# Kernel tuning notes

Hardware: AMD Instinct MI355X
Metric: run time of the kernel (lower is better)

## Reference

```python
import jax, jax.numpy as jnp
import numpy as np

B, N, E, D, L = 64, 128, 2048, 128, 4  # graphs, nodes/graph, edges/graph, channels, gnn layers
T = B * N  # total batched nodes


def setup_inputs() -> dict:
    key = jax.random.key(0)
    ks = jax.random.split(key, 16)
    s = 1.0 / np.sqrt(D)
    sc = 1.0 / np.sqrt(2 * D)
    inp = {
        "x": jax.random.normal(ks[0], (B, N, D), jnp.float32),
        "edges": jax.random.randint(ks[1], (B, 2, E), 0, N, dtype=jnp.int32),
        "Wg": jax.random.normal(ks[2], (L, D, D), jnp.float32) * s,
        "bg": jnp.zeros((L, D), jnp.float32),
        "Wq": jax.random.normal(ks[3], (D, D), jnp.float32) * s,
        "bq": jnp.zeros((D,), jnp.float32),
        "Wk": jax.random.normal(ks[4], (D, D), jnp.float32) * s,
        "bk": jnp.zeros((D,), jnp.float32),
        "Wv": jax.random.normal(ks[5], (D, D), jnp.float32) * s,
        "bv": jnp.zeros((D,), jnp.float32),
        "Wo": jax.random.normal(ks[6], (D, D), jnp.float32) * s,
        "bo": jnp.zeros((D,), jnp.float32),
        "Wc": jax.random.normal(ks[7], (2 * D, D), jnp.float32) * sc,
        "bc": jnp.zeros((D,), jnp.float32),
    }
    return inp


def _batched_edges(edges):
    # offset per-graph edge indices into the flat [T] node space, add self-loops
    off = (jnp.arange(B, dtype=edges.dtype) * N)[:, None]
    src = (edges[:, 0, :] + off).reshape(-1)
    dst = (edges[:, 1, :] + off).reshape(-1)
    loops = jnp.arange(T, dtype=edges.dtype)
    src = jnp.concatenate([src, loops])
    dst = jnp.concatenate([dst, loops])
    return src, dst


def reference(x, edges, Wg, bg, Wq, bq, Wk, bk, Wv, bv, Wo, bo, Wc, bc):
    xf = x.reshape(T, D)  # flat batched node features (torch_geo_batch.x)
    src, dst = _batched_edges(edges)
    # GCN symmetric normalization with self-loops: deg >= 1
    deg = jax.ops.segment_sum(jnp.ones(src.shape, xf.dtype), dst, num_segments=T)
    norm = jax.lax.rsqrt(deg)
    coef = (norm[src] * norm[dst])[:, None]
    # n_layers of GCNConv + tanh
    h = xf
    for l in range(L):
        m = h @ Wg[l]  # [T, D]
        h = jax.ops.segment_sum(m[src] * coef, dst, num_segments=T) + bg[l]
        h = jnp.tanh(h)
    batch_embedding = h.reshape(B, N, D)
    # DoubleHeadedAttention on the ORIGINAL batched input x; both inputs are
    # identical so the two attention heads compute the same tensor.
    q = xf @ Wq + bq
    k = xf @ Wk + bk
    v = xf @ Wv + bv
    attn = jax.nn.softmax(q @ k.T, axis=-1)  # [T, T]
    attended = (attn @ v) @ Wo + bo  # output_layer, == attended_input1 == attended_input2
    combined = jnp.concatenate([attended, attended], axis=-1)  # [T, 2D]
    att_output = combined @ Wc + bc  # combination_layer
    return jnp.concatenate([batch_embedding, att_output.reshape(B, N, D)], axis=-1)
```

## Files before the change

### kernel.cpp

```cpp
#include <hip/hip_runtime.h>
#include <math.h>

#define TT 8192
#define DD 128
#define GB 64
#define GN 128
#define GE 2048

#define WS_WG16    0u
#define WS_W2      (644u<<10)
#define WS_B2      (708u<<10)
#define WS_Q16     (1u<<20)
#define WS_K16     (3u<<20)
#define WS_VT      (5u<<20)
#define WS_OPART   (7u<<20)
#define WS_PM      (23u<<20)
#define WS_PL      ((23u<<20)+(256u<<10))

typedef _Float16 hfrag  __attribute__((ext_vector_type(8)));
typedef _Float16 h4     __attribute__((ext_vector_type(4)));
typedef float    ffrag  __attribute__((ext_vector_type(4)));

#define MFMA16(a,b,c) __builtin_amdgcn_mfma_f32_16x16x32_f16((a),(b),(c),0,0,0)

typedef __attribute__((address_space(1))) unsigned int gu32_t;
typedef __attribute__((address_space(3))) unsigned int lu32_t;
#define GLOAD16(gp, lp) __builtin_amdgcn_global_load_lds((gu32_t*)(const void*)(gp), (lu32_t*)(void*)(lp), 16, 0, 0)

__device__ __forceinline__ int fidx(int r_, int c_) {
  return (((r_>>4)*4 + (c_>>5))*64 + (r_&15) + 16*((c_>>3)&3))*8 + (c_&7);
}

__device__ __forceinline__ float tanh_fast(float x) {
  float e = __expf(2.f*x);
  return 1.f - 2.f/(e+1.f);
}

__global__ __launch_bounds__(512) void k_prep(const float* __restrict__ Wg,
                                              const float* __restrict__ Wo, const float* __restrict__ bo,
                                              const float* __restrict__ Wc, const float* __restrict__ bc,
                                              _Float16* __restrict__ wg16,
                                              float* __restrict__ W2, float* __restrict__ b2) {
  __shared__ float Wcs[128*128];
  const int tid = threadIdx.x;
  const int bid = blockIdx.x;
  if (bid < 4) {
    #pragma unroll
    for (int i=0;i<32;++i){
      int i2 = i*512 + tid;
      Wcs[i2] = Wc[i2] + Wc[i2 + 16384];
    }
    __syncthreads();
    const int r  = tid>>4;
    const int c0 = (tid&15)*8;
    const int ig = bid*32 + r;
    float acc[8];
    #pragma unroll
    for (int m=0;m<8;++m) acc[m]=0.f;
    for (int k=0;k<128;++k){
      float wo = Wo[ig*DD + k];
      #pragma unroll
      for (int m=0;m<8;++m) acc[m] += wo*Wcs[k*128 + c0 + m];
    }
    #pragma unroll
    for (int m=0;m<8;++m) W2[ig*DD + c0 + m] = acc[m];
    if (bid == 0){
      __syncthreads();
      if (tid < 128){
        float s = bc[tid];
        for (int k=0;k<128;++k) s += bo[k]*Wcs[k*128 + tid];
        b2[tid] = s;
      }
    }
  } else {
    const int l = bid - 4;
    const float* Wl = Wg + l*DD*DD;
    _Float16* dst = wg16 + l*16384;
    #pragma unroll
    for (int i=0;i<8;++i){
      int i4 = i*512 + tid;
      int k = i4>>5, i0 = (i4&31)<<2;
      float4 v = *(const float4*)&Wl[k*DD + i0];
      dst[fidx(i0+0,k)] = (_Float16)v.x;
      dst[fidx(i0+1,k)] = (_Float16)v.y;
      dst[fidx(i0+2,k)] = (_Float16)v.z;
      dst[fidx(i0+3,k)] = (_Float16)v.w;
    }
  }
}

__global__ __launch_bounds__(512,1) void fused_pre(
    const float* __restrict__ x, const int* __restrict__ edges,
    const _Float16* __restrict__ wg16, const float* __restrict__ bg,
    const float* __restrict__ Wq, const float* __restrict__ bq_,
    const float* __restrict__ Wk, const float* __restrict__ bk_,
    const float* __restrict__ Wv, const float* __restrict__ bv_,
    _Float16* __restrict__ q16, _Float16* __restrict__ k16, _Float16* __restrict__ vT,
    float* __restrict__ out)
{
  __shared__ __align__(16) char Lm[135168];
  const int tid  = threadIdx.x;
  const int bid  = blockIdx.x;

  if (bid < 64) {
    float*    Af   = (float*)Lm;
    _Float16* W16f = (_Float16*)Lm;
    _Float16* m16  = (_Float16*)(Lm + 32768);
    _Float16* h16  = (_Float16*)(Lm + 65536);
    _Float16* A16  = (_Float16*)(Lm + 98304);
    int*      cnt  = (int*)(Lm + 131072);
    float*    nrm  = (float*)(Lm + 131584);

    const int lane = tid & 63;
    const int w8   = tid >> 6;
    const int l15  = lane & 15;
    const int g    = lane >> 4;
    const int wi   = w8 >> 2;
    const int wj   = w8 & 3;
    const int b    = bid;
    const int* eg  = edges + b*2*GE;

    #pragma unroll
    for (int i=0;i<8;++i) ((float4*)Af)[i*512 + tid] = (float4){0.f,0.f,0.f,0.f};
    if (tid < 128) cnt[tid] = 0;
    __syncthreads();
    #pragma unroll
    for (int i=0;i<4;++i) atomicAdd(&cnt[eg[GE + i*512 + tid]], 1);
    __syncthreads();
    if (tid < 128) nrm[tid] = rsqrtf(1.f + (float)cnt[tid]);
    __syncthreads();
    #pragma unroll
    for (int i=0;i<4;++i){
      int s = eg[i*512 + tid], d = eg[GE + i*512 + tid];
      atomicAdd(&Af[d*128 + s], nrm[s]*nrm[d]);
    }
    __syncthreads();
    if (tid < 128) Af[tid*128 + tid] += nrm[tid]*nrm[tid];
    __syncthreads();
    #pragma unroll
    for (int i=0;i<8;++i){
      int i4 = i*512 + tid;
      float4 v = ((const float4*)Af)[i4];
      int dst = i4>>5, s4 = (i4&31)<<2;
      h4 t; t[0]=(_Float16)v.x; t[1]=(_Float16)v.y; t[2]=(_Float16)v.z; t[3]=(_Float16)v.w;
      *(h4*)&A16[fidx(dst, s4)] = t;
    }
    #pragma unroll
    for (int i=0;i<8;++i){
      int i4 = i*512 + tid;
      int n = i4>>5, k4 = (i4&31)<<2;
      float4 v = *(const float4*)&x[((size_t)b*128 + n)*128 + k4];
      h4 t; t[0]=(_Float16)v.x; t[1]=(_Float16)v.y; t[2]=(_Float16)v.z; t[3]=(_Float16)v.w;
      *(h4*)&h16[fidx(n, k4)] = t;
    }
    __syncthreads();
    #pragma unroll
    for (int i=0;i<4;++i){
      const int c = i*8 + w8;
      GLOAD16(wg16 + c*512 + lane*8, &W16f[c*512]);
    }
    asm volatile("s_waitcnt vmcnt(0)" ::: "memory");
    __syncthreads();

    for (int l=0; l<4; ++l){
      {
        hfrag bf[2][4];
        #pragma unroll
        for (int jj=0;jj<2;++jj){
          const int jg = wj*2+jj;
          #pragma unroll
          for (int ds=0;ds<4;++ds) bf[jj][ds] = *(const hfrag*)&h16[(jg*4+ds)*512 + lane*8];
        }
        #pragma unroll
        for (int it=0;it<4;++it){
          const int Ri = wi*4+it;
          hfrag af[4];
          #pragma unroll
          for (int ds=0;ds<4;++ds) af[ds] = *(const hfrag*)&W16f[(Ri*4+ds)*512 + lane*8];
          #pragma unroll
          for (int jj=0;jj<2;++jj){
            ffrag acc = (ffrag){0.f,0.f,0.f,0.f};
            #pragma unroll
            for (int ds=0;ds<4;++ds) acc = MFMA16(af[ds], bf[jj][ds], acc);
            const int src = (wj*2+jj)*16 + l15;
            const int sds = src>>5, s16 = 16*((src>>3)&3), s7 = src&7;
            #pragma unroll
            for (int r=0;r<4;++r)
              m16[((Ri*4 + sds)*64 + 4*g + r + s16)*8 + s7] = (_Float16)acc[r];
          }
        }
      }
      __syncthreads();
      if (l < 3){
        #pragma unroll
        for (int i=0;i<4;++i){
          const int c = i*8 + w8;
          GLOAD16(wg16 + (l+1)*16384 + c*512 + lane*8, &W16f[c*512]);
        }
      }
      {
        hfrag bf[2][4];
        float bgv[2];
        #pragma unroll
        for (int jj=0;jj<2;++jj){
          const int jg = wj*2+jj;
          #pragma unroll
          for (int ds=0;ds<4;++ds) bf[jj][ds] = *(const hfrag*)&m16[(jg*4+ds)*512 + lane*8];
          bgv[jj] = bg[l*DD + jg*16 + l15];
        }
        #pragma unroll
        for (int it=0;it<4;++it){
          const int Ri = wi*4+it;
          hfrag af[4];
          #pragma unroll
          for (int ds=0;ds<4;++ds) af[ds] = *(const hfrag*)&A16[(Ri*4+ds)*512 + lane*8];
          #pragma unroll
          for (int jj=0;jj<2;++jj){
            ffrag acc = (ffrag){0.f,0.f,0.f,0.f};
            #pragma unroll
            for (int ds=0;ds<4;++ds) acc = MFMA16(af[ds], bf[jj][ds], acc);
            const int dout = (wj*2+jj)*16 + l15;
            if (l < 3){
              const int dds = dout>>5, d16 = 16*((dout>>3)&3), d7 = dout&7;
              #pragma unroll
              for (int r=0;r<4;++r){
                float v = tanh_fast(acc[r] + bgv[jj]);
                h16[((Ri*4 + dds)*64 + 4*g + r + d16)*8 + d7] = (_Float16)v;
              }
            } else {
              #pragma unroll
              for (int r=0;r<4;++r){
                float v = tanh_fast(acc[r] + bgv[jj]);
                out[((size_t)b*128 + Ri*16 + 4*g + r)*(2*DD) + dout] = v;
              }
            }
          }
        }
      }
      __syncthreads();
    }
  } else {
    const int idx  = bid - 64;
    const int mode = idx >> 6;
    const int row0 = (idx & 63) * 128;
    const float* W    = (mode==0) ? Wq : (mode==1) ? Wk : Wv;
    const float* bias = (mode==0) ? bq_ : (mode==1) ? bk_ : bv_;
    float* Xs  = (float*)Lm;
    float* Ws2 = (float*)(Lm + 67584);

    #pragma unroll
    for (int i=0;i<8;++i){
      int i2 = i*512 + tid;
      int r = i2>>5, c4 = (i2&31)<<2;
      *(float4*)&Ws2[r*132+c4] = *(const float4*)&W[r*DD + c4];
      *(float4*)&Xs [r*132+c4] = *(const float4*)&x[(size_t)(row0+r)*DD + c4];
    }
    __syncthreads();

    const int r0 = (tid>>4)*4;
    const int cg = tid&15;
    const int c0 = cg*8;
    float acc[4][8];
    #pragma unroll
    for (int t=0;t<4;++t)
      #pragma unroll
      for (int m=0;m<8;++m) acc[t][m]=0.f;
    for (int kk=0;kk<128;kk+=4){
      float a[4][4];
      #pragma unroll
      for (int t=0;t<4;++t) *(float4*)a[t] = *(float4*)&Xs[(r0+t)*132+kk];
      #pragma unroll
      for (int j=0;j<4;++j){
        float w[8];
        *(float4*)&w[0] = *(float4*)&Ws2[(kk+j)*132+c0];
        *(float4*)&w[4] = *(float4*)&Ws2[(kk+j)*132+c0+4];
        #pragma unroll
        for (int t=0;t<4;++t)
          #pragma unroll
          for (int m=0;m<8;++m) acc[t][m] += a[t][j]*w[m];
      }
    }
    #pragma unroll
    for (int t=0;t<4;++t){
      const int row = row0 + r0 + t;
      float val[8];
      #pragma unroll
      for (int m=0;m<8;++m) val[m] = acc[t][m] + bias[c0+m];
      if (mode == 0) {
        hfrag h;
        #pragma unroll
        for (int m=0;m<8;++m) h[m] = (_Float16)val[m];
        *(hfrag*)&q16[(size_t)row*DD + c0] = h;
      } else if (mode == 1) {
        hfrag h;
        #pragma unroll
        for (int m=0;m<8;++m) h[m] = (_Float16)val[m];
        int R = row>>4, l15r = row&15, dsx = cg>>2, gx = cg&3;
        *(hfrag*)&k16[((size_t)(R*4+dsx)*64 + l15r + 16*gx)*8] = h;
      } else {
        int C = row>>5, kloc = row&31;
        int gx = (kloc&15)>>2;
        int jx = ((kloc>>4)<<2) | (kloc&3);
        #pragma unroll
        for (int m=0;m<8;++m){
          int d = c0+m;
          vT[((size_t)(C*8 + (d>>4))*64 + (d&15) + 16*gx)*8 + jx] = (_Float16)val[m];
        }
      }
    }
  }
}

__global__ __launch_bounds__(256,1) void k_flash5(
    const _Float16* __restrict__ q16, const _Float16* __restrict__ k16f,
    const _Float16* __restrict__ vTf,
    _Float16* __restrict__ Opart, float* __restrict__ pm, float* __restrict__ pl)
{
  __shared__ _Float16 Kb[2][8192];
  __shared__ _Float16 Vb[2][8192];
  const int tid  = threadIdx.x;
  const int lane = tid & 63;
  const int w4   = tid >> 6;
  const int l15  = lane & 15;
  const int g    = lane >> 4;
  const int qt   = blockIdx.x >> 3;
  const int sp   = blockIdx.x & 7;
  const int q0   = qt*256 + w4*64;

  hfrag qf[4][4];
  #pragma unroll
  for (int qb=0;qb<4;++qb)
    #pragma unroll
    for (int ds=0;ds<4;++ds)
      qf[qb][ds] = *(const hfrag*)&q16[(size_t)(q0+16*qb+l15)*DD + 32*ds + 8*g];

  float mrun[4] = {-1e30f,-1e30f,-1e30f,-1e30f}, lrun[4] = {0.f,0.f,0.f,0.f};
  ffrag o[4][8];
  #pragma unroll
  for (int qb=0;qb<4;++qb)
    #pragma unroll
    for (int nt=0;nt<8;++nt) o[qb][nt] = (ffrag){0.f,0.f,0.f,0.f};

  const size_t kbase = (size_t)(sp*1024)*DD;
  {
    const _Float16* Ks = k16f + kbase;
    const _Float16* Vs = vTf  + kbase;
    #pragma unroll
    for (int j=0;j<4;++j){
      const int c = w4*4 + j;
      GLOAD16(Ks + c*512 + lane*8, &Kb[0][c*512]);
      GLOAD16(Vs + c*512 + lane*8, &Vb[0][c*512]);
    }
  }
  __syncthreads();

  int cur = 0;
  for (int t=0; t<16; ++t){
    if (t < 15){
      const _Float16* Ks = k16f + kbase + (size_t)(t+1)*64*DD;
      const _Float16* Vs = vTf  + kbase + (size_t)(t+1)*64*DD;
      #pragma unroll
      for (int j=0;j<4;++j){
        const int c = w4*4 + j;
        GLOAD16(Ks + c*512 + lane*8, &Kb[cur^1][c*512]);
        GLOAD16(Vs + c*512 + lane*8, &Vb[cur^1][c*512]);
      }
    }

    ffrag s2[4][4];
    #pragma unroll
    for (int qb=0;qb<4;++qb)
      #pragma unroll
      for (int mt=0;mt<4;++mt) s2[qb][mt] = (ffrag){0.f,0.f,0.f,0.f};
    __builtin_amdgcn_s_setprio(1);
    #pragma unroll
    for (int mt=0;mt<4;++mt)
      #pragma unroll
      for (int ds=0;ds<4;++ds){
        hfrag kf = *(const hfrag*)&Kb[cur][(mt*4+ds)*512 + lane*8];
        #pragma unroll
        for (int qb=0;qb<4;++qb)
          s2[qb][mt] = MFMA16(kf, qf[qb][ds], s2[qb][mt]);
      }
    __builtin_amdgcn_s_setprio(0);

    #pragma unroll
    for (int qb=0;qb<4;++qb){
      float tmax = -1e30f;
      #pragma unroll
      for (int mt=0;mt<4;++mt)
        tmax = fmaxf(tmax, fmaxf(fmaxf(s2[qb][mt][0], s2[qb][mt][1]),
                                 fmaxf(s2[qb][mt][2], s2[qb][mt][3])));
      tmax = fmaxf(tmax, __shfl_xor(tmax,16));
      tmax = fmaxf(tmax, __shfl_xor(tmax,32));
      const float mnew = fmaxf(mrun[qb], tmax);
      float psum = 0.f;
      #pragma unroll
      for (int mt=0;mt<4;++mt)
        #pragma unroll
        for (int r=0;r<4;++r){ float e = __expf(s2[qb][mt][r]-mnew); s2[qb][mt][r]=e; psum += e; }
      psum += __shfl_xor(psum,16);
      psum += __shfl_xor(psum,32);
      if (__any(mnew > mrun[qb])){
        const float sc = __expf(mrun[qb]-mnew);
        lrun[qb] = lrun[qb]*sc + psum;
        mrun[qb] = mnew;
        #pragma unroll
        for (int r=0;r<4;++r){
          const float scr = __shfl(sc, 4*g+r);
          #pragma unroll
          for (int nt=0;nt<8;++nt) o[qb][nt][r] *= scr;
        }
      } else {
        lrun[qb] += psum;
      }
    }

    __builtin_amdgcn_s_setprio(1);
    #pragma unroll
    for (int c2=0;c2<2;++c2){
      hfrag pf[4];
      #pragma unroll
      for (int qb=0;qb<4;++qb)
        #pragma unroll
        for (int j=0;j<8;++j) pf[qb][j] = (_Float16)s2[qb][2*c2+(j>>2)][j&3];
      #pragma unroll
      for (int nt=0;nt<8;++nt){
        hfrag vf = *(const hfrag*)&Vb[cur][(c2*8+nt)*512 + lane*8];
        #pragma unroll
        for (int qb=0;qb<4;++qb)
          o[qb][nt] = MFMA16(pf[qb], vf, o[qb][nt]);
      }
    }
    __builtin_amdgcn_s_setprio(0);

    __syncthreads();
    cur ^= 1;
  }

  #pragma unroll
  for (int qb=0;qb<4;++qb){
    #pragma unroll
    for (int r=0;r<4;++r){
      _Float16* dst = &Opart[((size_t)sp*TT + q0 + 16*qb + 4*g + r)*DD];
      #pragma unroll
      for (int nt=0;nt<8;++nt)
        dst[16*nt + l15] = (_Float16)o[qb][nt][r];
    }
    if (g==0){
      pm[(size_t)sp*TT + q0 + 16*qb + l15] = mrun[qb];
      pl[(size_t)sp*TT + q0 + 16*qb + l15] = lrun[qb];
    }
  }
}

__global__ __launch_bounds__(256) void k_gemm_final(const _Float16* __restrict__ Opart,
                                                    const float* __restrict__ pm, const float* __restrict__ pl,
                                                    const float* __restrict__ W2, const float* __restrict__ b2,
                                                    float* __restrict__ out) {
  __shared__ float As[32*132];
  __shared__ float Ws[128*132];
  int tid = threadIdx.x;
  int row0 = blockIdx.x*32;
  #pragma unroll
  for (int i=0;i<4;i++){
    int idx = i*256+tid;
    int r = idx>>5, c4 = (idx&31)<<2;
    int t = row0 + r;
    float ms[8], ls[8];
    #pragma unroll
    for (int s=0;s<8;++s){ ms[s]=pm[(size_t)s*TT+t]; ls[s]=pl[(size_t)s*TT+t]; }
    float mx = ms[0];
    #pragma unroll
    for (int s=1;s<8;++s) mx = fmaxf(mx, ms[s]);
    float es[8]; float den = 0.f;
    #pragma unroll
    for (int s=0;s<8;++s){ es[s]=__expf(ms[s]-mx); den += ls[s]*es[s]; }
    float4 vv = {0.f,0.f,0.f,0.f};
    #pragma unroll
    for (int s=0;s<8;++s){
      float us = es[s]/den;
      h4 a = *(const h4*)&Opart[((size_t)s*TT + t)*DD + c4];
      vv.x += us*(float)a[0]; vv.y += us*(float)a[1];
      vv.z += us*(float)a[2]; vv.w += us*(float)a[3];
    }
    *(float4*)&As[r*132+c4] = vv;
  }
  #pragma unroll
  for (int i=0;i<16;i++){
    int idx = i*256+tid;
    int r = idx>>5, c4 = (idx&31)<<2;
    *(float4*)&Ws[r*132+c4] = *(const float4*)&W2[r*DD + c4];
  }
  __syncthreads();
  int rg = tid>>4, cg = tid&15;
  int r0 = rg*2, c0 = cg*8;
  float acc[2][8];
  #pragma unroll
  for (int a=0;a<2;a++)
    #pragma unroll
    for (int b=0;b<8;b++) acc[a][b]=0.f;
  for (int kk=0;kk<128;kk+=4){
    float a0[4], a1[4];
    *(float4*)a0 = *(float4*)&As[r0*132+kk];
    *(float4*)a1 = *(float4*)&As[(r0+1)*132+kk];
    #pragma unroll
    for (int j=0;j<4;j++){
      float w[8];
      *(float4*)&w[0] = *(float4*)&Ws[(kk+j)*132+c0];
      *(float4*)&w[4] = *(float4*)&Ws[(kk+j)*132+c0+4];
      #pragma unroll
      for (int m=0;m<8;m++){
        acc[0][m] += a0[j]*w[m];
        acc[1][m] += a1[j]*w[m];
      }
    }
  }
  #pragma unroll
  for (int a=0;a<2;a++){
    float outv[8];
    #pragma unroll
    for (int m=0;m<8;m++) outv[m] = acc[a][m] + b2[c0+m];
    float* dst = &out[(size_t)(row0+r0+a)*(2*DD) + DD + c0];
    *(float4*)&dst[0] = *(float4*)&outv[0];
    *(float4*)&dst[4] = *(float4*)&outv[4];
  }
}

extern "C" void kernel_launch(void* const* d_in, const int* in_sizes, int n_in,
                              void* d_out, int out_size, void* d_ws, size_t ws_size,
                              hipStream_t stream) {
  const float* x  = (const float*)d_in[0];
  const int* edges = (const int*)d_in[1];
  const float* Wg = (const float*)d_in[2];
  const float* bg = (const float*)d_in[3];
  const float* Wq = (const float*)d_in[4];
  const float* bq = (const float*)d_in[5];
  const float* Wk = (const float*)d_in[6];
  const float* bk = (const float*)d_in[7];
  const float* Wv = (const float*)d_in[8];
  const float* bv = (const float*)d_in[9];
  const float* Wo = (const float*)d_in[10];
  const float* bo = (const float*)d_in[11];
  const float* Wc = (const float*)d_in[12];
  const float* bc = (const float*)d_in[13];
  float* out = (float*)d_out;
  char* ws = (char*)d_ws;

  _Float16* wg16 = (_Float16*)(ws + WS_WG16);
  float* W2  = (float*)(ws + WS_W2);
  float* b2  = (float*)(ws + WS_B2);
  float* pm  = (float*)(ws + WS_PM);
  float* pl  = (float*)(ws + WS_PL);
  _Float16* Opart = (_Float16*)(ws + WS_OPART);
  _Float16* q16 = (_Float16*)(ws + WS_Q16);
  _Float16* k16 = (_Float16*)(ws + WS_K16);
  _Float16* vT  = (_Float16*)(ws + WS_VT);

  k_prep<<<8,512,0,stream>>>(Wg, Wo, bo, Wc, bc, wg16, W2, b2);
  fused_pre<<<256,512,0,stream>>>(x, edges, wg16, bg, Wq, bq, Wk, bk, Wv, bv,
                                  q16, k16, vT, out);
  k_flash5<<<256,256,0,stream>>>(q16, k16, vT, Opart, pm, pl);
  k_gemm_final<<<256,256,0,stream>>>(Opart, pm, pl, W2, b2, out);
}
```

Before: 122.2 us.

## Split flash attention block across 8 waves with 32 query rows each

The flash-attention kernel now launches 512 threads per block (8 waves) instead of 4, and each wave handles 32 query rows instead of 64. Per-wave register use for Q fragments, scores and output accumulators is halved, and the launch bound asks for 2 blocks per CU. The aim is more waves in flight to hide LDS and global-load latency. In exchange each K/V fragment read from LDS feeds only 2 MFMAs instead of 4, which doubles LDS read traffic per unit of compute.

```diff
diff --git a/kernel.cpp b/kernel.cpp
--- a/kernel.cpp
+++ b/kernel.cpp
@@ -311,7 +311,7 @@
   }
 }
 
-__global__ __launch_bounds__(256,1) void k_flash5(
+__global__ __launch_bounds__(512,2) void k_flash4(
     const _Float16* __restrict__ q16, const _Float16* __restrict__ k16f,
     const _Float16* __restrict__ vTf,
     _Float16* __restrict__ Opart, float* __restrict__ pm, float* __restrict__ pl)
@@ -320,24 +320,24 @@
   __shared__ _Float16 Vb[2][8192];
   const int tid  = threadIdx.x;
   const int lane = tid & 63;
-  const int w4   = tid >> 6;
+  const int w8   = tid >> 6;
   const int l15  = lane & 15;
   const int g    = lane >> 4;
   const int qt   = blockIdx.x >> 3;
   const int sp   = blockIdx.x & 7;
-  const int q0   = qt*256 + w4*64;
-
-  hfrag qf[4][4];
-  #pragma unroll
-  for (int qb=0;qb<4;++qb)
+  const int q0   = qt*256 + w8*32;
+
+  hfrag qf[2][4];
+  #pragma unroll
+  for (int qb=0;qb<2;++qb)
     #pragma unroll
     for (int ds=0;ds<4;++ds)
       qf[qb][ds] = *(const hfrag*)&q16[(size_t)(q0+16*qb+l15)*DD + 32*ds + 8*g];
 
-  float mrun[4] = {-1e30f,-1e30f,-1e30f,-1e30f}, lrun[4] = {0.f,0.f,0.f,0.f};
-  ffrag o[4][8];
-  #pragma unroll
-  for (int qb=0;qb<4;++qb)
+  float mrun[2] = {-1e30f,-1e30f}, lrun[2] = {0.f,0.f};
+  ffrag o[2][8];
+  #pragma unroll
+  for (int qb=0;qb<2;++qb)
     #pragma unroll
     for (int nt=0;nt<8;++nt) o[qb][nt] = (ffrag){0.f,0.f,0.f,0.f};
 
@@ -346,8 +346,8 @@
     const _Float16* Ks = k16f + kbase;
     const _Float16* Vs = vTf  + kbase;
     #pragma unroll
-    for (int j=0;j<4;++j){
-      const int c = w4*4 + j;
+    for (int j=0;j<2;++j){
+      const int c = w8*2 + j;
       GLOAD16(Ks + c*512 + lane*8, &Kb[0][c*512]);
       GLOAD16(Vs + c*512 + lane*8, &Vb[0][c*512]);
     }
@@ -360,16 +360,16 @@
       const _Float16* Ks = k16f + kbase + (size_t)(t+1)*64*DD;
       const _Float16* Vs = vTf  + kbase + (size_t)(t+1)*64*DD;
       #pragma unroll
-      for (int j=0;j<4;++j){
-        const int c = w4*4 + j;
+      for (int j=0;j<2;++j){
+        const int c = w8*2 + j;
         GLOAD16(Ks + c*512 + lane*8, &Kb[cur^1][c*512]);
         GLOAD16(Vs + c*512 + lane*8, &Vb[cur^1][c*512]);
       }
     }
 
-    ffrag s2[4][4];
-    #pragma unroll
-    for (int qb=0;qb<4;++qb)
+    ffrag s2[2][4];
+    #pragma unroll
+    for (int qb=0;qb<2;++qb)
       #pragma unroll
       for (int mt=0;mt<4;++mt) s2[qb][mt] = (ffrag){0.f,0.f,0.f,0.f};
     __builtin_amdgcn_s_setprio(1);
@@ -378,14 +378,13 @@
       #pragma unroll
       for (int ds=0;ds<4;++ds){
         hfrag kf = *(const hfrag*)&Kb[cur][(mt*4+ds)*512 + lane*8];
-        #pragma unroll
-        for (int qb=0;qb<4;++qb)
-          s2[qb][mt] = MFMA16(kf, qf[qb][ds], s2[qb][mt]);
+        s2[0][mt] = MFMA16(kf, qf[0][ds], s2[0][mt]);
+        s2[1][mt] = MFMA16(kf, qf[1][ds], s2[1][mt]);
       }
     __builtin_amdgcn_s_setprio(0);
 
     #pragma unroll
-    for (int qb=0;qb<4;++qb){
+    for (int qb=0;qb<2;++qb){
       float tmax = -1e30f;
       #pragma unroll
       for (int mt=0;mt<4;++mt)
@@ -419,17 +418,17 @@
     __builtin_amdgcn_s_setprio(1);
     #pragma unroll
     for (int c2=0;c2<2;++c2){
-      hfrag pf[4];
-      #pragma unroll
-      for (int qb=0;qb<4;++qb)
-        #pragma unroll
-        for (int j=0;j<8;++j) pf[qb][j] = (_Float16)s2[qb][2*c2+(j>>2)][j&3];
+      hfrag pf0, pf1;
+      #pragma unroll
+      for (int j=0;j<8;++j){
+        pf0[j] = (_Float16)s2[0][2*c2+(j>>2)][j&3];
+        pf1[j] = (_Float16)s2[1][2*c2+(j>>2)][j&3];
+      }
       #pragma unroll
       for (int nt=0;nt<8;++nt){
         hfrag vf = *(const hfrag*)&Vb[cur][(c2*8+nt)*512 + lane*8];
-        #pragma unroll
-        for (int qb=0;qb<4;++qb)
-          o[qb][nt] = MFMA16(pf[qb], vf, o[qb][nt]);
+        o[0][nt] = MFMA16(pf0, vf, o[0][nt]);
+        o[1][nt] = MFMA16(pf1, vf, o[1][nt]);
       }
     }
     __builtin_amdgcn_s_setprio(0);
@@ -439,7 +438,7 @@
   }
 
   #pragma unroll
-  for (int qb=0;qb<4;++qb){
+  for (int qb=0;qb<2;++qb){
     #pragma unroll
     for (int r=0;r<4;++r){
       _Float16* dst = &Opart[((size_t)sp*TT + q0 + 16*qb + 4*g + r)*DD];
@@ -560,6 +559,6 @@
   k_prep<<<8,512,0,stream>>>(Wg, Wo, bo, Wc, bc, wg16, W2, b2);
   fused_pre<<<256,512,0,stream>>>(x, edges, wg16, bg, Wq, bq, Wk, bk, Wv, bv,
                                   q16, k16, vT, out);
-  k_flash5<<<256,256,0,stream>>>(q16, k16, vT, Opart, pm, pl);
+  k_flash4<<<256,512,0,stream>>>(q16, k16, vT, Opart, pm, pl);
   k_gemm_final<<<256,256,0,stream>>>(Opart, pm, pl, W2, b2, out);
 }
```

After: 106.1 us. 1.15x faster.
